# Performance work log

Hardware: AMD Instinct MI355X
Metric: run time of the kernel (lower is better)

## Reference

```python
import jax, jax.numpy as jnp
import numpy as np

B, I, H = 8192, 2048, 2048


def setup_inputs() -> dict:
    key = jax.random.key(0)
    k = jax.random.split(key, 5)
    return {
        "x": jax.random.normal(k[0], (B, I), dtype=jnp.float32),
        "h_prev": jax.random.normal(k[1], (B, H), dtype=jnp.float32),
        "C_prev": jax.random.normal(k[2], (B, H), dtype=jnp.float32),
        # gate order along leading axis: f, i, C(tilde), o
        "W": jax.random.normal(k[3], (4, H, I), dtype=jnp.float32),
        "U": jax.random.normal(k[4], (4, H, H), dtype=jnp.float32),
        "b": jnp.zeros((4, H), dtype=jnp.float32),
    }


def reference(x, h_prev, C_prev, W, U, b):
    # Two fused GEMMs covering all 8 original matmuls, then one fused gate pass.
    # pre[g] = x @ W[g].T + h_prev @ U[g].T + b[g]   for g in (f, i, C~, o)
    pre = (jnp.einsum('bi,ghi->gbh', x, W)
           + jnp.einsum('bk,ghk->gbh', h_prev, U)
           + b[:, None, :])  # [4, B, H]
    f_t = jax.nn.sigmoid(pre[0])
    i_t = jax.nn.sigmoid(pre[1])
    C_tilda_t = jnp.tanh(pre[2])
    o_t = jax.nn.sigmoid(pre[3])
    C_t = f_t * C_prev + i_t * C_tilda_t
    h_t = o_t * jnp.tanh(C_t)
    # dynamics dict flattened into tuple: (input, forget, cell_update)
    return (h_t, C_t, i_t, f_t, C_tilda_t)
```

## Files before the change

kernel.cpp:

```cpp
#include <hip/hip_runtime.h>


#define PLANE 16777216
#define T_TILES 64

typedef _Float16 h8_t __attribute__((ext_vector_type(8)));
typedef _Float16 h4_t __attribute__((ext_vector_type(4)));
typedef float    f32x4 __attribute__((ext_vector_type(4)));

__device__ __forceinline__ float fast_sigmoid(float x) {
  return 1.0f / (1.0f + __expf(-x));
}
__device__ __forceinline__ float fast_tanh(float x) {
  float e = __expf(2.0f * x);
  return 1.0f - 2.0f / (e + 1.0f);
}

__global__ void split_hi_kernel(const float* __restrict__ src,
                                _Float16* __restrict__ hi, int n) {
  int idx = (blockIdx.x * blockDim.x + threadIdx.x) * 4;
  int stride = gridDim.x * blockDim.x * 4;
  for (int i = idx; i < n; i += stride) {
    float4 v = *reinterpret_cast<const float4*>(src + i);
    h4_t hv = {(_Float16)v.x, (_Float16)v.y, (_Float16)v.z, (_Float16)v.w};
    *reinterpret_cast<h4_t*>(hi + i) = hv;
  }
}

__device__ __forceinline__ void gload_lds16(const _Float16* g, _Float16* l) {
  __builtin_amdgcn_global_load_lds(
      (const __attribute__((address_space(1))) void*)g,
      (__attribute__((address_space(3))) void*)l, 16, 0, 0);
}

__device__ __forceinline__ const _Float16* segA(int kt,
    const _Float16* xH, const _Float16* hH) {
  return (kt >> 5) == 0 ? xH : hH;
}
__device__ __forceinline__ const _Float16* segB(int kt,
    const _Float16* wH, const _Float16* uH) {
  return (kt >> 5) == 0 ? wH : uH;
}
#define K0OF(kt) (((kt) & 31) << 6)

#define SYNC() do { __builtin_amdgcn_s_barrier();       \
                    __builtin_amdgcn_sched_barrier(0); } while (0)

__global__ __launch_bounds__(512, 2) void gemm_gates_kernel(
    const _Float16* __restrict__ xH, const _Float16* __restrict__ hH,
    const _Float16* __restrict__ wH, const _Float16* __restrict__ uH,
    const float* __restrict__ bias,
    float* __restrict__ out, _Float16* __restrict__ o_ws) {
  __shared__ _Float16 sA[2][256 * 64];
  __shared__ _Float16 sB[2][256 * 64];

  const int bid = blockIdx.x;
  const int wg = (bid & 7) * 128 + (bid >> 3);
  const int tm = wg >> 5;
  const int tn = wg & 31;
  const int rowA = tm * 256;
  const int rowB = tn * 256;

  const int tid = threadIdx.x;
  const int w = tid >> 6;
  const int lane = tid & 63;
  const int wr = w >> 2;
  const int wc = w & 3;

  const int lrow = lane & 15;
  const int q = lane >> 4;
  const int swl = (lane & 7) << 4;
  const int co0 = (((0 << 6) | (q << 4)) ^ swl) >> 1;
  const int co1 = (((1 << 6) | (q << 4)) ^ swl) >> 1;

  f32x4 acc[8][4];
#pragma unroll
  for (int m = 0; m < 8; ++m)
#pragma unroll
    for (int n = 0; n < 4; ++n)
      acc[m][n] = (f32x4){0.f, 0.f, 0.f, 0.f};

  size_t aOff[2][2], bOff[2][2];
  int ldsOff[2];
#pragma unroll
  for (int j = 0; j < 2; ++j) {
    const int c = j * 512 + tid;
    const int r = c >> 3;
    const int sw = ((c & 7) << 4) ^ ((r & 7) << 4);
    ldsOff[j] = c * 8;
#pragma unroll
    for (int hh = 0; hh < 2; ++hh) {
      aOff[hh][j] = (size_t)(rowA + hh * 128 + r) * 2048 + (sw >> 1);
      bOff[hh][j] = (size_t)(rowB + hh * 128 + r) * 2048 + (sw >> 1);
    }
  }

#define STAGE_A(kt, hh) do {                                             \
    const _Float16* sg = segA((kt), xH, hH);                             \
    const size_t k0 = (size_t)K0OF(kt);                                  \
    _Float16* d = sA[(kt) & 1] + (hh) * 8192;                            \
    gload_lds16(sg + aOff[hh][0] + k0, d + ldsOff[0]);                   \
    gload_lds16(sg + aOff[hh][1] + k0, d + ldsOff[1]);                   \
  } while (0)
#define STAGE_B(kt, hh) do {                                             \
    const _Float16* sg = segB((kt), wH, uH);                             \
    const size_t k0 = (size_t)K0OF(kt);                                  \
    _Float16* d = sB[(kt) & 1] + (hh) * 8192;                            \
    gload_lds16(sg + bOff[hh][0] + k0, d + ldsOff[0]);                   \
    gload_lds16(sg + bOff[hh][1] + k0, d + ldsOff[1]);                   \
  } while (0)

  STAGE_A(0, 0); STAGE_A(0, 1); STAGE_B(0, 0); STAGE_B(0, 1);
  STAGE_A(1, 0); STAGE_A(1, 1); STAGE_B(1, 0);

  h8_t aLo[4][2], aHi[4][2];
  h8_t bN01[2][2], bN23[2][2];

  for (int t = 0; t < T_TILES; ++t) {
    const _Float16* aP = sA[t & 1];
    const _Float16* bP = sB[t & 1];

    if (t == T_TILES - 1) { asm volatile("s_waitcnt vmcnt(0)"); }
    else                  { asm volatile("s_waitcnt vmcnt(6)"); }
    SYNC();

#pragma unroll
    for (int m = 0; m < 4; ++m) {
      const _Float16* rp = aP + (wr * 128 + m * 16 + lrow) * 64;
      aLo[m][0] = *reinterpret_cast<const h8_t*>(rp + co0);
      aLo[m][1] = *reinterpret_cast<const h8_t*>(rp + co1);
    }
#pragma unroll
    for (int nn = 0; nn < 2; ++nn) {
      const _Float16* rp = bP + (wc * 64 + nn * 16 + lrow) * 64;
      bN01[nn][0] = *reinterpret_cast<const h8_t*>(rp + co0);
      bN01[nn][1] = *reinterpret_cast<const h8_t*>(rp + co1);
    }
    if (t + 1 < T_TILES) STAGE_B(t + 1, 1);
    SYNC();
    __builtin_amdgcn_s_setprio(1);
#pragma unroll
    for (int mm = 0; mm < 4; ++mm)
#pragma unroll
      for (int nn = 0; nn < 2; ++nn)
#pragma unroll
        for (int kk = 0; kk < 2; ++kk)
          acc[mm][nn] = __builtin_amdgcn_mfma_f32_16x16x32_f16(
              aLo[mm][kk], bN01[nn][kk], acc[mm][nn], 0, 0, 0);
    __builtin_amdgcn_s_setprio(0);
    SYNC();

#pragma unroll
    for (int m = 0; m < 4; ++m) {
      const _Float16* rp = aP + (wr * 128 + (4 + m) * 16 + lrow) * 64;
      aHi[m][0] = *reinterpret_cast<const h8_t*>(rp + co0);
      aHi[m][1] = *reinterpret_cast<const h8_t*>(rp + co1);
    }
    SYNC();
    __builtin_amdgcn_s_setprio(1);
#pragma unroll
    for (int mm = 0; mm < 4; ++mm)
#pragma unroll
      for (int nn = 0; nn < 2; ++nn)
#pragma unroll
        for (int kk = 0; kk < 2; ++kk)
          acc[4 + mm][nn] = __builtin_amdgcn_mfma_f32_16x16x32_f16(
              aHi[mm][kk], bN01[nn][kk], acc[4 + mm][nn], 0, 0, 0);
    __builtin_amdgcn_s_setprio(0);
    SYNC();

#pragma unroll
    for (int nn = 0; nn < 2; ++nn) {
      const _Float16* rp = bP + (wc * 64 + (2 + nn) * 16 + lrow) * 64;
      bN23[nn][0] = *reinterpret_cast<const h8_t*>(rp + co0);
      bN23[nn][1] = *reinterpret_cast<const h8_t*>(rp + co1);
    }
    if (t + 2 < T_TILES) { STAGE_A(t + 2, 0); STAGE_A(t + 2, 1); }
    SYNC();
    __builtin_amdgcn_s_setprio(1);
#pragma unroll
    for (int mm = 0; mm < 4; ++mm)
#pragma unroll
      for (int nn = 0; nn < 2; ++nn)
#pragma unroll
        for (int kk = 0; kk < 2; ++kk)
          acc[mm][2 + nn] = __builtin_amdgcn_mfma_f32_16x16x32_f16(
              aLo[mm][kk], bN23[nn][kk], acc[mm][2 + nn], 0, 0, 0);
    __builtin_amdgcn_s_setprio(0);
    SYNC();

    if (t + 2 < T_TILES) STAGE_B(t + 2, 0);
    SYNC();
    __builtin_amdgcn_s_setprio(1);
#pragma unroll
    for (int mm = 0; mm < 4; ++mm)
#pragma unroll
      for (int nn = 0; nn < 2; ++nn)
#pragma unroll
        for (int kk = 0; kk < 2; ++kk)
          acc[4 + mm][2 + nn] = __builtin_amdgcn_mfma_f32_16x16x32_f16(
              aHi[mm][kk], bN23[nn][kk], acc[4 + mm][2 + nn], 0, 0, 0);
    __builtin_amdgcn_s_setprio(0);
  }

  const int gate = tn >> 3;
  const int row0 = tm * 256 + wr * 128 + (lane >> 4) * 4;
  const int col0 = tn * 256 + wc * 64 + (lane & 15);
#pragma unroll
  for (int n = 0; n < 4; ++n) {
    const int col = col0 + n * 16;
    const int hcol = col & 2047;
    const float bv = bias[col];
#pragma unroll
    for (int m = 0; m < 8; ++m) {
      const int row = row0 + m * 16;
#pragma unroll
      for (int r = 0; r < 4; ++r) {
        float v = acc[m][n][r] + bv;
        size_t oidx = (size_t)(row + r) * 2048 + hcol;
        if (gate == 0)       out[(size_t)3 * PLANE + oidx] = fast_sigmoid(v);
        else if (gate == 1)  out[(size_t)2 * PLANE + oidx] = fast_sigmoid(v);
        else if (gate == 2)  out[(size_t)4 * PLANE + oidx] = fast_tanh(v);
        else                 o_ws[oidx] = (_Float16)fast_sigmoid(v);
      }
    }
  }
}

__global__ void final_kernel(const float* __restrict__ outr,
                             const float* __restrict__ C_prev,
                             const _Float16* __restrict__ o_ws,
                             float* __restrict__ out) {
  const float* iP = outr + (size_t)2 * PLANE;
  const float* fP = outr + (size_t)3 * PLANE;
  const float* cP = outr + (size_t)4 * PLANE;
  int idx = (blockIdx.x * blockDim.x + threadIdx.x) * 4;
  int stride = gridDim.x * blockDim.x * 4;
  for (int i = idx; i < PLANE; i += stride) {
    float4 fv = *reinterpret_cast<const float4*>(fP + i);
    float4 iv = *reinterpret_cast<const float4*>(iP + i);
    float4 cv = *reinterpret_cast<const float4*>(cP + i);
    float4 cp = *reinterpret_cast<const float4*>(C_prev + i);
    h4_t ov = *reinterpret_cast<const h4_t*>(o_ws + i);
    float4 C, H;
    C.x = fv.x * cp.x + iv.x * cv.x;
    C.y = fv.y * cp.y + iv.y * cv.y;
    C.z = fv.z * cp.z + iv.z * cv.z;
    C.w = fv.w * cp.w + iv.w * cv.w;
    H.x = (float)ov.x * fast_tanh(C.x);
    H.y = (float)ov.y * fast_tanh(C.y);
    H.z = (float)ov.z * fast_tanh(C.z);
    H.w = (float)ov.w * fast_tanh(C.w);
    *reinterpret_cast<float4*>(out + (size_t)PLANE + i) = C;
    *reinterpret_cast<float4*>(out + i) = H;
  }
}

extern "C" void kernel_launch(void* const* d_in, const int* in_sizes, int n_in,
                              void* d_out, int out_size, void* d_ws, size_t ws_size,
                              hipStream_t stream) {
  const float* x  = (const float*)d_in[0];
  const float* hp = (const float*)d_in[1];
  const float* Cp = (const float*)d_in[2];
  const float* W  = (const float*)d_in[3];
  const float* U  = (const float*)d_in[4];
  const float* b  = (const float*)d_in[5];
  float* out = (float*)d_out;

  _Float16* ws = (_Float16*)d_ws;
  _Float16* xh = ws;
  _Float16* hh = xh + PLANE;
  _Float16* Wh = hh + PLANE;
  _Float16* Uh = Wh + PLANE;
  _Float16* o_ws = Uh + PLANE;

  dim3 blk(256);
  split_hi_kernel<<<dim3(2048), blk, 0, stream>>>(x, xh, PLANE);
  split_hi_kernel<<<dim3(2048), blk, 0, stream>>>(hp, hh, PLANE);
  split_hi_kernel<<<dim3(2048), blk, 0, stream>>>(W, Wh, PLANE);
  split_hi_kernel<<<dim3(2048), blk, 0, stream>>>(U, Uh, PLANE);
  gemm_gates_kernel<<<dim3(1024), dim3(512), 0, stream>>>(xh, hh, Wh, Uh,
                                                          b, out, o_ws);
  final_kernel<<<dim3(2048), blk, 0, stream>>>(out, Cp, o_ws, out);
}
```

Measured before the change: 925.3 us.

## Interleave gate rows in weights and fuse cell update into GEMM epilogue

Weight matrices are permuted during fp16 conversion so that the four gate columns for each hidden unit sit adjacent in the GEMM output. The epilogue then exchanges gate activations across neighbouring lanes with shuffles and computes C_t and h_t directly. This removes the separate final elementwise kernel, its re-reads of the f/i/C~ planes and the fp16 o workspace. In exchange, only one lane in four performs the C/h writes, the gate-plane stores become strided (stride-4 column mapping), and C_prev reads are uncoalesced.

New measurement: 1.131 ms. 1.22x slower.

```diff
diff --git a/kernel.cpp b/kernel.cpp
--- a/kernel.cpp
+++ b/kernel.cpp
@@ -27,6 +27,22 @@
   }
 }
 
+__global__ void split_permute_kernel(const float* __restrict__ src,
+                                     _Float16* __restrict__ dst, int n) {
+  int idx = (blockIdx.x * blockDim.x + threadIdx.x) * 4;
+  int stride = gridDim.x * blockDim.x * 4;
+  for (int i = idx; i < n; i += stride) {
+    float4 v = *reinterpret_cast<const float4*>(src + i);
+    const int k = i & 2047;
+    const int gh = i >> 11;
+    const int g = gh >> 11;
+    const int h = gh & 2047;
+    const size_t d = ((size_t)(h * 4 + g) << 11) + k;
+    h4_t hv = {(_Float16)v.x, (_Float16)v.y, (_Float16)v.z, (_Float16)v.w};
+    *reinterpret_cast<h4_t*>(dst + d) = hv;
+  }
+}
+
 __device__ __forceinline__ void gload_lds16(const _Float16* g, _Float16* l) {
   __builtin_amdgcn_global_load_lds(
       (const __attribute__((address_space(1))) void*)g,
@@ -38,8 +54,8 @@
   return (kt >> 5) == 0 ? xH : hH;
 }
 __device__ __forceinline__ const _Float16* segB(int kt,
-    const _Float16* wH, const _Float16* uH) {
-  return (kt >> 5) == 0 ? wH : uH;
+    const _Float16* wP, const _Float16* uP) {
+  return (kt >> 5) == 0 ? wP : uP;
 }
 #define K0OF(kt) (((kt) & 31) << 6)
 
@@ -48,9 +64,9 @@
 
 __global__ __launch_bounds__(512, 2) void gemm_gates_kernel(
     const _Float16* __restrict__ xH, const _Float16* __restrict__ hH,
-    const _Float16* __restrict__ wH, const _Float16* __restrict__ uH,
-    const float* __restrict__ bias,
-    float* __restrict__ out, _Float16* __restrict__ o_ws) {
+    const _Float16* __restrict__ wP, const _Float16* __restrict__ uP,
+    const float* __restrict__ bias, const float* __restrict__ C_prev,
+    float* __restrict__ out) {
   __shared__ _Float16 sA[2][256 * 64];
   __shared__ _Float16 sB[2][256 * 64];
 
@@ -103,7 +119,7 @@
     gload_lds16(sg + aOff[hh][1] + k0, d + ldsOff[1]);                   \
   } while (0)
 #define STAGE_B(kt, hh) do {                                             \
-    const _Float16* sg = segB((kt), wH, uH);                             \
+    const _Float16* sg = segB((kt), wP, uP);                             \
     const size_t k0 = (size_t)K0OF(kt);                                  \
     _Float16* d = sB[(kt) & 1] + (hh) * 8192;                            \
     gload_lds16(sg + bOff[hh][0] + k0, d + ldsOff[0]);                   \
@@ -203,56 +219,35 @@
     __builtin_amdgcn_s_setprio(0);
   }
 
-  const int gate = tn >> 3;
   const int row0 = tm * 256 + wr * 128 + (lane >> 4) * 4;
   const int col0 = tn * 256 + wc * 64 + (lane & 15);
+  const int gsel = col0 & 3;
 #pragma unroll
   for (int n = 0; n < 4; ++n) {
     const int col = col0 + n * 16;
-    const int hcol = col & 2047;
-    const float bv = bias[col];
+    const int hcol = col >> 2;
+    const float bv = bias[gsel * 2048 + hcol];
 #pragma unroll
     for (int m = 0; m < 8; ++m) {
       const int row = row0 + m * 16;
 #pragma unroll
       for (int r = 0; r < 4; ++r) {
-        float v = acc[m][n][r] + bv;
-        size_t oidx = (size_t)(row + r) * 2048 + hcol;
-        if (gate == 0)       out[(size_t)3 * PLANE + oidx] = fast_sigmoid(v);
-        else if (gate == 1)  out[(size_t)2 * PLANE + oidx] = fast_sigmoid(v);
-        else if (gate == 2)  out[(size_t)4 * PLANE + oidx] = fast_tanh(v);
-        else                 o_ws[oidx] = (_Float16)fast_sigmoid(v);
+        const size_t oidx = (size_t)(row + r) * 2048 + hcol;
+        const float v = acc[m][n][r] + bv;
+        const float a = (gsel == 2) ? fast_tanh(v) : fast_sigmoid(v);
+        if (gsel == 0)      out[(size_t)3 * PLANE + oidx] = a;
+        else if (gsel == 1) out[(size_t)2 * PLANE + oidx] = a;
+        else if (gsel == 2) out[(size_t)4 * PLANE + oidx] = a;
+        const float a1 = __shfl_xor(a, 1);
+        const float a2 = __shfl_xor(a, 2);
+        const float a3 = __shfl_xor(a, 3);
+        if (gsel == 0) {
+          const float C = a * C_prev[oidx] + a1 * a2;
+          out[(size_t)PLANE + oidx] = C;
+          out[oidx] = a3 * fast_tanh(C);
+        }
       }
     }
-  }
-}
-
-__global__ void final_kernel(const float* __restrict__ outr,
-                             const float* __restrict__ C_prev,
-                             const _Float16* __restrict__ o_ws,
-                             float* __restrict__ out) {
-  const float* iP = outr + (size_t)2 * PLANE;
-  const float* fP = outr + (size_t)3 * PLANE;
-  const float* cP = outr + (size_t)4 * PLANE;
-  int idx = (blockIdx.x * blockDim.x + threadIdx.x) * 4;
-  int stride = gridDim.x * blockDim.x * 4;
-  for (int i = idx; i < PLANE; i += stride) {
-    float4 fv = *reinterpret_cast<const float4*>(fP + i);
-    float4 iv = *reinterpret_cast<const float4*>(iP + i);
-    float4 cv = *reinterpret_cast<const float4*>(cP + i);
-    float4 cp = *reinterpret_cast<const float4*>(C_prev + i);
-    h4_t ov = *reinterpret_cast<const h4_t*>(o_ws + i);
-    float4 C, H;
-    C.x = fv.x * cp.x + iv.x * cv.x;
-    C.y = fv.y * cp.y + iv.y * cv.y;
-    C.z = fv.z * cp.z + iv.z * cv.z;
-    C.w = fv.w * cp.w + iv.w * cv.w;
-    H.x = (float)ov.x * fast_tanh(C.x);
-    H.y = (float)ov.y * fast_tanh(C.y);
-    H.z = (float)ov.z * fast_tanh(C.z);
-    H.w = (float)ov.w * fast_tanh(C.w);
-    *reinterpret_cast<float4*>(out + (size_t)PLANE + i) = C;
-    *reinterpret_cast<float4*>(out + i) = H;
   }
 }
 
@@ -270,16 +265,14 @@
   _Float16* ws = (_Float16*)d_ws;
   _Float16* xh = ws;
   _Float16* hh = xh + PLANE;
-  _Float16* Wh = hh + PLANE;
-  _Float16* Uh = Wh + PLANE;
-  _Float16* o_ws = Uh + PLANE;
+  _Float16* Wp = hh + PLANE;
+  _Float16* Up = Wp + PLANE;
 
   dim3 blk(256);
   split_hi_kernel<<<dim3(2048), blk, 0, stream>>>(x, xh, PLANE);
   split_hi_kernel<<<dim3(2048), blk, 0, stream>>>(hp, hh, PLANE);
-  split_hi_kernel<<<dim3(2048), blk, 0, stream>>>(W, Wh, PLANE);
-  split_hi_kernel<<<dim3(2048), blk, 0, stream>>>(U, Uh, PLANE);
-  gemm_gates_kernel<<<dim3(1024), dim3(512), 0, stream>>>(xh, hh, Wh, Uh,
-                                                          b, out, o_ws);
-  final_kernel<<<dim3(2048), blk, 0, stream>>>(out, Cp, o_ws, out);
-}
+  split_permute_kernel<<<dim3(2048), blk, 0, stream>>>(W, Wp, PLANE);
+  split_permute_kernel<<<dim3(2048), blk, 0, stream>>>(U, Up, PLANE);
+  gemm_gates_kernel<<<dim3(1024), dim3(512), 0, stream>>>(xh, hh, Wp, Up,
+                                                          b, Cp, out);
+}
```
